# Performance work log

Hardware: AMD Instinct MI355X
Metric: run time of the kernel (lower is better)

## Reference

```python
import jax, jax.numpy as jnp
import numpy as np

B, D, A, H, NH = 32768, 768, 17, 128, 4
DH = H // NH


def _ln(x, g, b, eps=1e-5):
    mu = jnp.mean(x, axis=-1, keepdims=True)
    var = jnp.mean((x - mu) ** 2, axis=-1, keepdims=True)
    return (x - mu) / jnp.sqrt(var + eps) * g + b


def setup_inputs() -> dict:
    key = jax.random.key(0)
    ks = jax.random.split(key, 16)
    s = 0.02
    return {
        "visual_feat": jax.random.normal(ks[0], (B, D), jnp.float32),
        "au_feat": jax.random.uniform(ks[1], (B, A), jnp.float32),
        "w_tok": jax.random.normal(ks[2], (H, 1), jnp.float32) * s,
        "b_tok": jnp.zeros((H,), jnp.float32),
        "pos": jax.random.normal(ks[3], (1, A, H), jnp.float32) * s,
        "g_auln": jnp.ones((H,), jnp.float32),
        "b_auln": jnp.zeros((H,), jnp.float32),
        "w_q": jax.random.normal(ks[4], (H, D), jnp.float32) * s,
        "b_q": jnp.zeros((H,), jnp.float32),
        "w_in": jax.random.normal(ks[5], (3 * H, H), jnp.float32) * s,  # packed q,k,v in_proj
        "b_in": jnp.zeros((3 * H,), jnp.float32),
        "w_ao": jax.random.normal(ks[6], (H, H), jnp.float32) * s,  # MHA out_proj
        "b_ao": jnp.zeros((H,), jnp.float32),
        "g_aln": jnp.ones((H,), jnp.float32),
        "b_aln": jnp.zeros((H,), jnp.float32),
        "w_out": jax.random.normal(ks[7], (D, H), jnp.float32) * s,
        "b_out": jnp.zeros((D,), jnp.float32),
        "w_gate": jax.random.normal(ks[8], (D, 2 * D), jnp.float32) * s,
        "b_gate": jnp.zeros((D,), jnp.float32),
    }


def reference(visual_feat, au_feat, w_tok, b_tok, pos, g_auln, b_auln,
              w_q, b_q, w_in, b_in, w_ao, b_ao, g_aln, b_aln,
              w_out, b_out, w_gate, b_gate):
    # AU tokens: Linear(1 -> H) on intensities, + pos embed, LN. [B, A, H]
    au_tokens = au_feat[..., None] * w_tok[:, 0] + b_tok
    au_tokens = _ln(au_tokens + pos, g_auln, b_auln)
    # query: [B, H] (seq len 1)
    query = visual_feat @ w_q.T + b_q
    # MultiheadAttention (batch_first, packed in_proj)
    wq, wk, wv = w_in[:H], w_in[H:2 * H], w_in[2 * H:]
    bq, bk, bv = b_in[:H], b_in[H:2 * H], b_in[2 * H:]
    q = (query @ wq.T + bq).reshape(-1, NH, DH)          # [B, nh, dh]
    k = (au_tokens @ wk.T + bk).reshape(-1, A, NH, DH)   # [B, A, nh, dh]
    v = (au_tokens @ wv.T + bv).reshape(-1, A, NH, DH)
    scale = 1.0 / jnp.sqrt(jnp.asarray(DH, q.dtype))
    scores = jnp.einsum('bhd,bahd->bha', q * scale, k)   # [B, nh, A]
    attn = jax.nn.softmax(scores, axis=-1)
    ctx = jnp.einsum('bha,bahd->bhd', attn, v).reshape(-1, H)
    attn_out = ctx @ w_ao.T + b_ao
    attn_out = _ln(attn_out, g_aln, b_aln)
    attn_feat = attn_out @ w_out.T + b_out               # [B, D]
    gate_in = jnp.concatenate([visual_feat, attn_feat], axis=1)
    gate = jax.nn.sigmoid(gate_in @ w_gate.T + b_gate)
    return gate * attn_feat + (1.0 - gate) * visual_feat
```

## Files before the change

kernel.cpp:

```cpp
#include <hip/hip_runtime.h>
#include <hip/hip_bf16.h>

typedef __hip_bfloat16 bf16;
typedef __attribute__((ext_vector_type(8))) short short8;
typedef __attribute__((ext_vector_type(4))) float f32x4;
typedef __attribute__((ext_vector_type(8))) __bf16 bf16x8;

#define NB 32768
#define DD 768
#define AA 17
#define HH 128

__device__ __forceinline__ float bs2f(short s){
  unsigned int u = ((unsigned int)(unsigned short)s) << 16;
  return __builtin_bit_cast(float, u);
}
__device__ __forceinline__ short f2bs(float f){
  bf16 h = __float2bfloat16(f);
  return __builtin_bit_cast(short, h);
}
__device__ __forceinline__ f32x4 mfma16(short8 a, short8 b, f32x4 c){
  return __builtin_amdgcn_mfma_f32_16x16x32_bf16(
      __builtin_bit_cast(bf16x8, a), __builtin_bit_cast(bf16x8, b), c, 0, 0, 0);
}

template<int F32>
__device__ __forceinline__ short8 ldchunk(const void* base, long elem_off){
  if (F32){
    const float4* p = (const float4*)((const float*)base + elem_off);
    float4 x = p[0], y = p[1];
    short8 r;
    r[0]=f2bs(x.x); r[1]=f2bs(x.y); r[2]=f2bs(x.z); r[3]=f2bs(x.w);
    r[4]=f2bs(y.x); r[5]=f2bs(y.y); r[6]=f2bs(y.z); r[7]=f2bs(y.w);
    return r;
  } else {
    return *(const short8*)((const short*)base + elem_off);
  }
}


__device__ __forceinline__ float blk_mean128(float v, float* tmp){
  int t = threadIdx.x;
  #pragma unroll
  for (int m = 32; m; m >>= 1) v += __shfl_xor(v, m);
  if ((t & 63) == 0) tmp[t >> 6] = v;
  __syncthreads();
  float r = (tmp[0] + tmp[1]) * (1.0f / 128.0f);
  __syncthreads();
  return r;
}

__global__ void prep1(const float* __restrict__ w_tok, const float* __restrict__ b_tok,
                      const float* __restrict__ pos, const float* __restrict__ g_auln,
                      float* __restrict__ ug, float* __restrict__ rg, float* __restrict__ coef){
  __shared__ float tmp[2];
  int h = threadIdx.x;
  float w = w_tok[h];
  float wbar = blk_mean128(w, tmp);
  float u = w - wbar;
  float g = g_auln[h];
  ug[h] = u * g;
  float muu = blk_mean128(u * u, tmp);
  if (h == 0) coef[0] = muu;
  float bt = b_tok[h];
  for (int a = 0; a < AA; ++a){
    float c = bt + pos[a * HH + h];
    float cbar = blk_mean128(c, tmp);
    float r = c - cbar;
    rg[a * HH + h] = r * g;
    float mur = blk_mean128(u * r, tmp);
    float mrr = blk_mean128(r * r, tmp);
    if (h == 0){ coef[1 + a] = mur; coef[18 + a] = mrr; }
  }
}

__global__ void prep2(const float* __restrict__ w_in, const float* __restrict__ b_in,
                      const float* __restrict__ b_auln, const float* __restrict__ b_q,
                      const float* __restrict__ ug, const float* __restrict__ rg,
                      float* __restrict__ Uk, float* __restrict__ Ck,
                      float* __restrict__ Uv, float* __restrict__ Cv,
                      float* __restrict__ Rk, float* __restrict__ Rv,
                      float* __restrict__ bqf){
  int hp = threadIdx.x, bid = blockIdx.x;
  const float* wqrow = w_in + (long)hp * HH;
  const float* wkrow = w_in + (long)(HH + hp) * HH;
  const float* wvrow = w_in + (long)(2 * HH + hp) * HH;
  if (bid < AA){
    int a = bid;
    float sk = 0.f, sv = 0.f;
    for (int t = 0; t < HH; ++t){
      float r = rg[a * HH + t];
      sk += r * wkrow[t];
      sv += r * wvrow[t];
    }
    Rk[a * HH + hp] = sk; Rv[a * HH + hp] = sv;
  } else if (bid == AA){
    float uk = 0.f, uv = 0.f, ck = 0.f, cv = 0.f;
    for (int t = 0; t < HH; ++t){
      float u = ug[t], ba = b_auln[t];
      float wk = wkrow[t], wv = wvrow[t];
      uk += u * wk; uv += u * wv; ck += ba * wk; cv += ba * wv;
    }
    Uk[hp] = uk; Uv[hp] = uv;
    Ck[hp] = ck + b_in[HH + hp];
    Cv[hp] = cv + b_in[2 * HH + hp];
  } else {
    float s = 0.f;
    for (int t = 0; t < HH; ++t) s += b_q[t] * wqrow[t];
    bqf[hp] = s + b_in[hp];
  }
}

__global__ void prep_wqf(const float* __restrict__ w_in, const float* __restrict__ w_q,
                         bf16* __restrict__ Wqf){
  __shared__ float wq[HH];
  int h = blockIdx.x, t = threadIdx.x;
  if (t < HH) wq[t] = w_in[(long)h * HH + t];
  __syncthreads();
  for (int j = t; j < DD; j += 256){
    float acc = 0.f;
    for (int k = 0; k < HH; ++k) acc += wq[k] * w_q[(long)k * DD + j];
    Wqf[(long)h * DD + j] = __float2bfloat16(acc);
  }
}

__global__ void prep_gate(const float* __restrict__ w_gate, const float* __restrict__ b_gate,
                          const float* __restrict__ w_out, const float* __restrict__ b_out,
                          bf16* __restrict__ Wg1b, bf16* __restrict__ Wg2w,
                          bf16* __restrict__ Woutb, float* __restrict__ bgp){
  __shared__ float wg2[DD];
  __shared__ float red[2];
  int c = blockIdx.x, t = threadIdx.x;
  const float* wrow = w_gate + (long)c * (2 * DD);
  for (int j = t; j < DD; j += 128){
    Wg1b[(long)c * DD + j] = __float2bfloat16(wrow[j]);
    wg2[j] = wrow[DD + j];
  }
  __syncthreads();
  float acc = 0.f;
  for (int j = 0; j < DD; ++j) acc = fmaf(wg2[j], w_out[(long)j * HH + t], acc);
  Wg2w[(long)c * HH + t] = __float2bfloat16(acc);
  Woutb[(long)c * HH + t] = __float2bfloat16(w_out[(long)c * HH + t]);
  float pb = 0.f;
  for (int j = t; j < DD; j += 128) pb = fmaf(wg2[j], b_out[j], pb);
  #pragma unroll
  for (int m = 32; m; m >>= 1) pb += __shfl_xor(pb, m);
  if ((t & 63) == 0) red[t >> 6] = pb;
  __syncthreads();
  if (t == 0) bgp[c] = b_gate[c] + red[0] + red[1];
}

__global__ __launch_bounds__(128) void attn(
    const bf16* __restrict__ Q, const float* __restrict__ au, const float* __restrict__ coef,
    const float* __restrict__ Uk_, const float* __restrict__ Ck_,
    const float* __restrict__ Uv_, const float* __restrict__ Cv_,
    const float* __restrict__ Rk, const float* __restrict__ Rv,
    bf16* __restrict__ ctx){
  const int ROWS = 8;
  int h = threadIdx.x;
  long row0 = (long)blockIdx.x * ROWS;
  float Uk = Uk_[h], Ck = Ck_[h], Uv = Uv_[h], Cv = Cv_[h];
  float cA = coef[0];
  __shared__ float sa[ROWS * AA];
  for (int idx = h; idx < ROWS * AA; idx += 128)
    sa[idx] = au[row0 * AA + idx];
  __syncthreads();
  const float scale = 0.17677669529663689f;
  for (int r = 0; r < ROWS; ++r){
    long row = row0 + r;
    float q = __bfloat162float(Q[row * HH + h]);
    float sc[AA], vv[AA];
    #pragma unroll
    for (int a = 0; a < AA; ++a){
      float s = sa[r * AA + a];
      float var = fmaf(s * s, cA, fmaf(2.f * s, coef[1 + a], coef[18 + a]));
      float rinv = rsqrtf(fmaxf(var, 0.f) + 1e-5f);
      float kk = fmaf(s, Uk, Rk[a * HH + h]) * rinv + Ck;
      vv[a]    = fmaf(s, Uv, Rv[a * HH + h]) * rinv + Cv;
      float p = q * kk;
      p += __shfl_xor(p, 16); p += __shfl_xor(p, 8); p += __shfl_xor(p, 4);
      p += __shfl_xor(p, 2);  p += __shfl_xor(p, 1);
      sc[a] = p * scale;
    }
    float mx = sc[0];
    #pragma unroll
    for (int a = 1; a < AA; ++a) mx = fmaxf(mx, sc[a]);
    float den = 0.f, cval = 0.f;
    #pragma unroll
    for (int a = 0; a < AA; ++a){
      float e = __expf(sc[a] - mx);
      den += e; cval += e * vv[a];
    }
    ctx[row * HH + h] = __float2bfloat16(cval / den);
  }
}

template<int MODE, int AF, int BF, int SIDE>
__global__ __launch_bounds__(256) void gemm_bt(
    const void* __restrict__ A, long lda, int ks,
    const void* __restrict__ Bw, long ldb,
    const float* __restrict__ bias,
    const float* __restrict__ g_ln, const float* __restrict__ b_ln,
    short* __restrict__ sideA,
    bf16* __restrict__ C, long ldc)
{
  __shared__ __align__(16) short smem[128 * 136];
  short* As = smem;
  short* Bs = smem + 5120;
  const int tid = threadIdx.x;
  const int w = tid >> 6, l = tid & 63;
  const long rowBase = (long)blockIdx.y * 128;
  const int colBase = blockIdx.x * 128;
  const int fr = l & 15;
  const int kq = l >> 4;
  const int sr0 = tid >> 2,         sp0 = (tid & 3) * 8;
  const int sr1 = (tid + 256) >> 2;

  f32x4 acc[2][8];
  f32x4 zero = {0.f, 0.f, 0.f, 0.f};
  #pragma unroll
  for (int i = 0; i < 2; ++i)
    #pragma unroll
    for (int j = 0; j < 8; ++j) acc[i][j] = zero;

  for (int kt = 0; kt < ks; ++kt){
    const long kA = (long)kt * 32;
    short8 av0 = ldchunk<AF>(A, (rowBase + sr0) * lda + kA + sp0);
    short8 av1 = ldchunk<AF>(A, (rowBase + sr1) * lda + kA + sp0);
    short8 bv0 = ldchunk<BF>(Bw, (long)(colBase + sr0) * ldb + kA + sp0);
    short8 bv1 = ldchunk<BF>(Bw, (long)(colBase + sr1) * ldb + kA + sp0);
    if (SIDE){
      *(short8*)(sideA + (rowBase + sr0) * lda + kA + sp0) = av0;
      *(short8*)(sideA + (rowBase + sr1) * lda + kA + sp0) = av1;
    }
    __syncthreads();
    *(short8*)(As + sr0 * 40 + sp0) = av0;
    *(short8*)(As + sr1 * 40 + sp0) = av1;
    *(short8*)(Bs + sr0 * 40 + sp0) = bv0;
    *(short8*)(Bs + sr1 * 40 + sp0) = bv1;
    __syncthreads();
    const int ra0 = w * 32 + fr;
    short8 a0 = *(const short8*)(As + ra0 * 40 + kq * 8);
    short8 a1 = *(const short8*)(As + (ra0 + 16) * 40 + kq * 8);
    #pragma unroll
    for (int nt = 0; nt < 8; ++nt){
      short8 b = *(const short8*)(Bs + (nt * 16 + fr) * 40 + kq * 8);
      acc[0][nt] = mfma16(a0, b, acc[0][nt]);
      acc[1][nt] = mfma16(a1, b, acc[1][nt]);
    }
  }
  __syncthreads();

  short* ep = smem;
  if (MODE == 1){
    #pragma unroll
    for (int mt = 0; mt < 2; ++mt){
      #pragma unroll
      for (int r = 0; r < 4; ++r){
        float x[8]; float sm = 0.f, sq = 0.f;
        #pragma unroll
        for (int nt = 0; nt < 8; ++nt){
          const int col = colBase + nt * 16 + fr;
          x[nt] = acc[mt][nt][r] + bias[col];
          sm += x[nt]; sq += x[nt] * x[nt];
        }
        sm += __shfl_xor(sm, 1); sq += __shfl_xor(sq, 1);
        sm += __shfl_xor(sm, 2); sq += __shfl_xor(sq, 2);
        sm += __shfl_xor(sm, 4); sq += __shfl_xor(sq, 4);
        sm += __shfl_xor(sm, 8); sq += __shfl_xor(sq, 8);
        const float mu = sm * (1.f / 128.f);
        const float var = sq * (1.f / 128.f) - mu * mu;
        const float rinv = rsqrtf(fmaxf(var, 0.f) + 1e-5f);
        const int lrow = w * 32 + mt * 16 + kq * 4 + r;
        #pragma unroll
        for (int nt = 0; nt < 8; ++nt){
          const int col = colBase + nt * 16 + fr;
          float y = (x[nt] - mu) * rinv * g_ln[col] + b_ln[col];
          ep[lrow * 136 + nt * 16 + fr] = f2bs(y);
        }
      }
    }
  } else {
    #pragma unroll
    for (int nt = 0; nt < 8; ++nt){
      const int col = colBase + nt * 16 + fr;
      const float bv = bias[col];
      #pragma unroll
      for (int mt = 0; mt < 2; ++mt){
        const int lrow0 = w * 32 + mt * 16 + kq * 4;
        #pragma unroll
        for (int r = 0; r < 4; ++r)
          ep[(lrow0 + r) * 136 + nt * 16 + fr] = f2bs(acc[mt][nt][r] + bv);
      }
    }
  }
  __syncthreads();

  #pragma unroll
  for (int it = 0; it < 8; ++it){
    const int cid = tid + it * 256;
    const int rw = cid >> 4;
    const int cc = (cid & 15) * 8;
    const long gr = rowBase + rw;
    short8 vls = *(const short8*)(ep + rw * 136 + cc);
    short* cp = (short*)C + gr * ldc + colBase + cc;
    *(short8*)cp = vls;
  }
}

template<int A1F>
__global__ __launch_bounds__(256) void gemm_final(
    const void* __restrict__ A1,
    const bf16* __restrict__ aon,
    const bf16* __restrict__ Wg1b,
    const bf16* __restrict__ Wg2w,
    const bf16* __restrict__ Woutb,
    const float* __restrict__ bgp,
    const float* __restrict__ b_out,
    const float* __restrict__ vf,
    float* __restrict__ C)
{
  __shared__ __align__(16) short As[128 * 40];
  __shared__ __align__(16) short Bs[128 * 40];
  __shared__ __align__(16) short Bs2[128 * 40];
  const int tid = threadIdx.x;
  const int w = tid >> 6, l = tid & 63;
  const long rowBase = (long)blockIdx.y * 128;
  const int colBase = blockIdx.x * 128;
  const int fr = l & 15;
  const int kq = l >> 4;
  const int sr0 = tid >> 2,         sp0 = (tid & 3) * 8;
  const int sr1 = (tid + 256) >> 2;

  f32x4 accG[2][8], accF[2][8];
  f32x4 zero = {0.f, 0.f, 0.f, 0.f};
  #pragma unroll
  for (int i = 0; i < 2; ++i)
    #pragma unroll
    for (int j = 0; j < 8; ++j){ accG[i][j] = zero; accF[i][j] = zero; }

  for (int kt = 0; kt < DD / 32; ++kt){
    const long kA = (long)kt * 32;
    short8 av0 = ldchunk<A1F>(A1, (rowBase + sr0) * DD + kA + sp0);
    short8 av1 = ldchunk<A1F>(A1, (rowBase + sr1) * DD + kA + sp0);
    short8 bv0 = *(const short8*)((const short*)Wg1b + (long)(colBase + sr0) * DD + kA + sp0);
    short8 bv1 = *(const short8*)((const short*)Wg1b + (long)(colBase + sr1) * DD + kA + sp0);
    __syncthreads();
    *(short8*)(As + sr0 * 40 + sp0) = av0;
    *(short8*)(As + sr1 * 40 + sp0) = av1;
    *(short8*)(Bs + sr0 * 40 + sp0) = bv0;
    *(short8*)(Bs + sr1 * 40 + sp0) = bv1;
    __syncthreads();
    const int ra0 = w * 32 + fr;
    short8 a0 = *(const short8*)(As + ra0 * 40 + kq * 8);
    short8 a1 = *(const short8*)(As + (ra0 + 16) * 40 + kq * 8);
    #pragma unroll
    for (int nt = 0; nt < 8; ++nt){
      short8 b = *(const short8*)(Bs + (nt * 16 + fr) * 40 + kq * 8);
      accG[0][nt] = mfma16(a0, b, accG[0][nt]);
      accG[1][nt] = mfma16(a1, b, accG[1][nt]);
    }
  }

  for (int kt = 0; kt < HH / 32; ++kt){
    const long kA = (long)kt * 32;
    short8 av0 = *(const short8*)((const short*)aon + (rowBase + sr0) * HH + kA + sp0);
    short8 av1 = *(const short8*)((const short*)aon + (rowBase + sr1) * HH + kA + sp0);
    short8 bv0 = *(const short8*)((const short*)Wg2w + (long)(colBase + sr0) * HH + kA + sp0);
    short8 bv1 = *(const short8*)((const short*)Wg2w + (long)(colBase + sr1) * HH + kA + sp0);
    short8 cv0 = *(const short8*)((const short*)Woutb + (long)(colBase + sr0) * HH + kA + sp0);
    short8 cv1 = *(const short8*)((const short*)Woutb + (long)(colBase + sr1) * HH + kA + sp0);
    __syncthreads();
    *(short8*)(As + sr0 * 40 + sp0) = av0;
    *(short8*)(As + sr1 * 40 + sp0) = av1;
    *(short8*)(Bs + sr0 * 40 + sp0) = bv0;
    *(short8*)(Bs + sr1 * 40 + sp0) = bv1;
    *(short8*)(Bs2 + sr0 * 40 + sp0) = cv0;
    *(short8*)(Bs2 + sr1 * 40 + sp0) = cv1;
    __syncthreads();
    const int ra0 = w * 32 + fr;
    short8 a0 = *(const short8*)(As + ra0 * 40 + kq * 8);
    short8 a1 = *(const short8*)(As + (ra0 + 16) * 40 + kq * 8);
    #pragma unroll
    for (int nt = 0; nt < 8; ++nt){
      short8 b  = *(const short8*)(Bs  + (nt * 16 + fr) * 40 + kq * 8);
      short8 b2 = *(const short8*)(Bs2 + (nt * 16 + fr) * 40 + kq * 8);
      accG[0][nt] = mfma16(a0, b,  accG[0][nt]);
      accG[1][nt] = mfma16(a1, b,  accG[1][nt]);
      accF[0][nt] = mfma16(a0, b2, accF[0][nt]);
      accF[1][nt] = mfma16(a1, b2, accF[1][nt]);
    }
  }

  float bg[8], bo[8];
  #pragma unroll
  for (int nt = 0; nt < 8; ++nt){
    const int col = colBase + nt * 16 + fr;
    bg[nt] = bgp[col];
    bo[nt] = b_out[col];
  }
  #pragma unroll
  for (int mt = 0; mt < 2; ++mt){
    const long r0 = rowBase + w * 32 + mt * 16 + kq * 4;
    #pragma unroll
    for (int r = 0; r < 4; ++r){
      const long row = r0 + r;
      const float* vrow = vf + row * DD;
      float* crow = C + row * DD;
      #pragma unroll
      for (int nt = 0; nt < 8; ++nt){
        const int col = colBase + nt * 16 + fr;
        const float lin = accG[mt][nt][r] + bg[nt];
        const float afv = accF[mt][nt][r] + bo[nt];
        const float gate = 1.f / (1.f + __expf(-lin));
        crow[col] = gate * afv + (1.f - gate) * vrow[col];
      }
    }
  }
}

extern "C" void kernel_launch(void* const* d_in, const int* in_sizes, int n_in,
                              void* d_out, int out_size, void* d_ws, size_t ws_size,
                              hipStream_t stream){
  const float* visual = (const float*)d_in[0];
  const float* au     = (const float*)d_in[1];
  const float* w_tok  = (const float*)d_in[2];
  const float* b_tok  = (const float*)d_in[3];
  const float* pos    = (const float*)d_in[4];
  const float* g_auln = (const float*)d_in[5];
  const float* b_auln = (const float*)d_in[6];
  const float* w_q    = (const float*)d_in[7];
  const float* b_q    = (const float*)d_in[8];
  const float* w_in   = (const float*)d_in[9];
  const float* b_in   = (const float*)d_in[10];
  const float* w_ao   = (const float*)d_in[11];
  const float* b_ao   = (const float*)d_in[12];
  const float* g_aln  = (const float*)d_in[13];
  const float* b_aln  = (const float*)d_in[14];
  const float* w_out  = (const float*)d_in[15];
  const float* b_out  = (const float*)d_in[16];
  const float* w_gate = (const float*)d_in[17];
  const float* b_gate = (const float*)d_in[18];

  char* ob = (char*)d_out;
  bf16* Q   = (bf16*)(ob);
  bf16* ctx = (bf16*)(ob + ((size_t)8 << 20));
  char* p = ob + ((size_t)16 << 20);
  auto alloc = [&](size_t bytes){ char* r = p; p += (bytes + 255) & ~(size_t)255; return r; };
  bf16*  Wqf  = (bf16*) alloc((size_t)HH * DD * 2);
  float* bqf  = (float*)alloc(HH * 4);
  float* ug   = (float*)alloc(HH * 4);
  float* rg   = (float*)alloc(AA * HH * 4);
  float* coef = (float*)alloc(64 * 4);
  float* Uk   = (float*)alloc(HH * 4);
  float* Ck   = (float*)alloc(HH * 4);
  float* Uv   = (float*)alloc(HH * 4);
  float* Cv   = (float*)alloc(HH * 4);
  float* Rk   = (float*)alloc(AA * HH * 4);
  float* Rv   = (float*)alloc(AA * HH * 4);

  char* q = (char*)d_ws;
  auto walloc = [&](size_t bytes){ char* r = q; q += (bytes + 255) & ~(size_t)255; return r; };
  bf16*  aon   = (bf16*) walloc((size_t)NB * HH * 2);
  bf16*  Wg1b  = (bf16*) walloc((size_t)DD * DD * 2);
  bf16*  Wg2w  = (bf16*) walloc((size_t)DD * HH * 2);
  bf16*  Woutb = (bf16*) walloc((size_t)DD * HH * 2);
  float* bgp   = (float*)walloc(DD * 4);
  bf16*  vbf   = (bf16*) walloc((size_t)NB * DD * 2);
  const bool use_vbf = (size_t)(q - (char*)d_ws) <= ws_size;

  prep1<<<dim3(1), dim3(128), 0, stream>>>(w_tok, b_tok, pos, g_auln, ug, rg, coef);
  prep2<<<dim3(19), dim3(128), 0, stream>>>(w_in, b_in, b_auln, b_q, ug, rg, Uk, Ck, Uv, Cv, Rk, Rv, bqf);
  prep_wqf<<<dim3(128), dim3(256), 0, stream>>>(w_in, w_q, Wqf);
  prep_gate<<<dim3(DD), dim3(128), 0, stream>>>(w_gate, b_gate, w_out, b_out, Wg1b, Wg2w, Woutb, bgp);

  if (use_vbf)
    gemm_bt<0, 1, 0, 1><<<dim3(1, NB / 128), dim3(256), 0, stream>>>(
        visual, (long)DD, DD / 32, Wqf, (long)DD,
        bqf, nullptr, nullptr, (short*)vbf, Q, (long)HH);
  else
    gemm_bt<0, 1, 0, 0><<<dim3(1, NB / 128), dim3(256), 0, stream>>>(
        visual, (long)DD, DD / 32, Wqf, (long)DD,
        bqf, nullptr, nullptr, nullptr, Q, (long)HH);

  attn<<<dim3(NB / 8), dim3(128), 0, stream>>>(Q, au, coef, Uk, Ck, Uv, Cv, Rk, Rv, ctx);

  gemm_bt<1, 0, 1, 0><<<dim3(1, NB / 128), dim3(256), 0, stream>>>(
      ctx, (long)HH, HH / 32, w_ao, (long)HH,
      b_ao, g_aln, b_aln, nullptr, aon, (long)HH);

  if (use_vbf)
    gemm_final<0><<<dim3(DD / 128, NB / 128), dim3(256), 0, stream>>>(
        vbf, aon, Wg1b, Wg2w, Woutb, bgp, b_out, visual, (float*)d_out);
  else
    gemm_final<1><<<dim3(DD / 128, NB / 128), dim3(256), 0, stream>>>(
        visual, aon, Wg1b, Wg2w, Woutb, bgp, b_out, visual, (float*)d_out);
}
```

Baseline: 532.7 us.

## Double-buffer LDS tiles in GEMM kernels and add XCD-aware block swizzle

Both GEMM kernels now use two LDS tile buffers. Each iteration prefetches the next K-slice from global memory into registers while MFMAs run on the current buffer, then writes the prefetched data into the other buffer, so only one barrier is needed per iteration instead of two. This is meant to hide global-load latency behind compute. gemm_final also remaps block IDs so that blocks dispatched round-robin to the same XCD cover contiguous rows, which should improve L2 reuse of A rows. In exchange it uses more LDS and registers, which may lower occupancy.

```diff
diff --git a/kernel.cpp b/kernel.cpp
--- a/kernel.cpp
+++ b/kernel.cpp
@@ -204,9 +204,7 @@
     short* __restrict__ sideA,
     bf16* __restrict__ C, long ldc)
 {
-  __shared__ __align__(16) short smem[128 * 136];
-  short* As = smem;
-  short* Bs = smem + 5120;
+  __shared__ __align__(16) short smem[20480];
   const int tid = threadIdx.x;
   const int w = tid >> 6, l = tid & 63;
   const long rowBase = (long)blockIdx.y * 128;
@@ -223,30 +221,52 @@
     #pragma unroll
     for (int j = 0; j < 8; ++j) acc[i][j] = zero;
 
+  {
+    short8 av0 = ldchunk<AF>(A, (rowBase + sr0) * lda + sp0);
+    short8 av1 = ldchunk<AF>(A, (rowBase + sr1) * lda + sp0);
+    short8 bv0 = ldchunk<BF>(Bw, (long)(colBase + sr0) * ldb + sp0);
+    short8 bv1 = ldchunk<BF>(Bw, (long)(colBase + sr1) * ldb + sp0);
+    if (SIDE){
+      *(short8*)(sideA + (rowBase + sr0) * lda + sp0) = av0;
+      *(short8*)(sideA + (rowBase + sr1) * lda + sp0) = av1;
+    }
+    *(short8*)(smem + sr0 * 40 + sp0) = av0;
+    *(short8*)(smem + sr1 * 40 + sp0) = av1;
+    *(short8*)(smem + 5120 + sr0 * 40 + sp0) = bv0;
+    *(short8*)(smem + 5120 + sr1 * 40 + sp0) = bv1;
+  }
+
   for (int kt = 0; kt < ks; ++kt){
-    const long kA = (long)kt * 32;
-    short8 av0 = ldchunk<AF>(A, (rowBase + sr0) * lda + kA + sp0);
-    short8 av1 = ldchunk<AF>(A, (rowBase + sr1) * lda + kA + sp0);
-    short8 bv0 = ldchunk<BF>(Bw, (long)(colBase + sr0) * ldb + kA + sp0);
-    short8 bv1 = ldchunk<BF>(Bw, (long)(colBase + sr1) * ldb + kA + sp0);
-    if (SIDE){
-      *(short8*)(sideA + (rowBase + sr0) * lda + kA + sp0) = av0;
-      *(short8*)(sideA + (rowBase + sr1) * lda + kA + sp0) = av1;
-    }
     __syncthreads();
-    *(short8*)(As + sr0 * 40 + sp0) = av0;
-    *(short8*)(As + sr1 * 40 + sp0) = av1;
-    *(short8*)(Bs + sr0 * 40 + sp0) = bv0;
-    *(short8*)(Bs + sr1 * 40 + sp0) = bv1;
-    __syncthreads();
+    short* cb = smem + (kt & 1) * 10240;
+    short* nb = smem + ((kt + 1) & 1) * 10240;
+    const bool pf = (kt + 1 < ks);
+    short8 av0, av1, bv0, bv1;
+    if (pf){
+      const long kA = (long)(kt + 1) * 32;
+      av0 = ldchunk<AF>(A, (rowBase + sr0) * lda + kA + sp0);
+      av1 = ldchunk<AF>(A, (rowBase + sr1) * lda + kA + sp0);
+      bv0 = ldchunk<BF>(Bw, (long)(colBase + sr0) * ldb + kA + sp0);
+      bv1 = ldchunk<BF>(Bw, (long)(colBase + sr1) * ldb + kA + sp0);
+      if (SIDE){
+        *(short8*)(sideA + (rowBase + sr0) * lda + kA + sp0) = av0;
+        *(short8*)(sideA + (rowBase + sr1) * lda + kA + sp0) = av1;
+      }
+    }
     const int ra0 = w * 32 + fr;
-    short8 a0 = *(const short8*)(As + ra0 * 40 + kq * 8);
-    short8 a1 = *(const short8*)(As + (ra0 + 16) * 40 + kq * 8);
+    short8 a0 = *(const short8*)(cb + ra0 * 40 + kq * 8);
+    short8 a1 = *(const short8*)(cb + (ra0 + 16) * 40 + kq * 8);
     #pragma unroll
     for (int nt = 0; nt < 8; ++nt){
-      short8 b = *(const short8*)(Bs + (nt * 16 + fr) * 40 + kq * 8);
+      short8 b = *(const short8*)(cb + 5120 + (nt * 16 + fr) * 40 + kq * 8);
       acc[0][nt] = mfma16(a0, b, acc[0][nt]);
       acc[1][nt] = mfma16(a1, b, acc[1][nt]);
+    }
+    if (pf){
+      *(short8*)(nb + sr0 * 40 + sp0) = av0;
+      *(short8*)(nb + sr1 * 40 + sp0) = av1;
+      *(short8*)(nb + 5120 + sr0 * 40 + sp0) = bv0;
+      *(short8*)(nb + 5120 + sr1 * 40 + sp0) = bv1;
     }
   }
   __syncthreads();
@@ -320,13 +340,17 @@
     const float* __restrict__ vf,
     float* __restrict__ C)
 {
-  __shared__ __align__(16) short As[128 * 40];
-  __shared__ __align__(16) short Bs[128 * 40];
-  __shared__ __align__(16) short Bs2[128 * 40];
+  __shared__ __align__(16) short smem[20480];
   const int tid = threadIdx.x;
   const int w = tid >> 6, l = tid & 63;
-  const long rowBase = (long)blockIdx.y * 128;
-  const int colBase = blockIdx.x * 128;
+
+  const int nx = 6;
+  const int bid = blockIdx.y * nx + blockIdx.x;
+  const int cpx = (NB / 128) * nx / 8;
+  const int swz = (bid & 7) * cpx + (bid >> 3);
+  const long rowBase = (long)(swz / nx) * 128;
+  const int colBase = (swz % nx) * 128;
+
   const int fr = l & 15;
   const int kq = l >> 4;
   const int sr0 = tid >> 2,         sp0 = (tid & 3) * 8;
@@ -339,29 +363,49 @@
     #pragma unroll
     for (int j = 0; j < 8; ++j){ accG[i][j] = zero; accF[i][j] = zero; }
 
+  {
+    short8 av0 = ldchunk<A1F>(A1, (rowBase + sr0) * DD + sp0);
+    short8 av1 = ldchunk<A1F>(A1, (rowBase + sr1) * DD + sp0);
+    short8 bv0 = *(const short8*)((const short*)Wg1b + (long)(colBase + sr0) * DD + sp0);
+    short8 bv1 = *(const short8*)((const short*)Wg1b + (long)(colBase + sr1) * DD + sp0);
+    *(short8*)(smem + sr0 * 40 + sp0) = av0;
+    *(short8*)(smem + sr1 * 40 + sp0) = av1;
+    *(short8*)(smem + 5120 + sr0 * 40 + sp0) = bv0;
+    *(short8*)(smem + 5120 + sr1 * 40 + sp0) = bv1;
+  }
   for (int kt = 0; kt < DD / 32; ++kt){
-    const long kA = (long)kt * 32;
-    short8 av0 = ldchunk<A1F>(A1, (rowBase + sr0) * DD + kA + sp0);
-    short8 av1 = ldchunk<A1F>(A1, (rowBase + sr1) * DD + kA + sp0);
-    short8 bv0 = *(const short8*)((const short*)Wg1b + (long)(colBase + sr0) * DD + kA + sp0);
-    short8 bv1 = *(const short8*)((const short*)Wg1b + (long)(colBase + sr1) * DD + kA + sp0);
     __syncthreads();
-    *(short8*)(As + sr0 * 40 + sp0) = av0;
-    *(short8*)(As + sr1 * 40 + sp0) = av1;
-    *(short8*)(Bs + sr0 * 40 + sp0) = bv0;
-    *(short8*)(Bs + sr1 * 40 + sp0) = bv1;
-    __syncthreads();
+    short* cb = smem + (kt & 1) * 10240;
+    short* nb = smem + ((kt + 1) & 1) * 10240;
+    const bool pf = (kt + 1 < DD / 32);
+    short8 av0, av1, bv0, bv1;
+    if (pf){
+      const long kA = (long)(kt + 1) * 32;
+      av0 = ldchunk<A1F>(A1, (rowBase + sr0) * DD + kA + sp0);
+      av1 = ldchunk<A1F>(A1, (rowBase + sr1) * DD + kA + sp0);
+      bv0 = *(const short8*)((const short*)Wg1b + (long)(colBase + sr0) * DD + kA + sp0);
+      bv1 = *(const short8*)((const short*)Wg1b + (long)(colBase + sr1) * DD + kA + sp0);
+    }
     const int ra0 = w * 32 + fr;
-    short8 a0 = *(const short8*)(As + ra0 * 40 + kq * 8);
-    short8 a1 = *(const short8*)(As + (ra0 + 16) * 40 + kq * 8);
+    short8 a0 = *(const short8*)(cb + ra0 * 40 + kq * 8);
+    short8 a1 = *(const short8*)(cb + (ra0 + 16) * 40 + kq * 8);
     #pragma unroll
     for (int nt = 0; nt < 8; ++nt){
-      short8 b = *(const short8*)(Bs + (nt * 16 + fr) * 40 + kq * 8);
+      short8 b = *(const short8*)(cb + 5120 + (nt * 16 + fr) * 40 + kq * 8);
       accG[0][nt] = mfma16(a0, b, accG[0][nt]);
       accG[1][nt] = mfma16(a1, b, accG[1][nt]);
     }
-  }
-
+    if (pf){
+      *(short8*)(nb + sr0 * 40 + sp0) = av0;
+      *(short8*)(nb + sr1 * 40 + sp0) = av1;
+      *(short8*)(nb + 5120 + sr0 * 40 + sp0) = bv0;
+      *(short8*)(nb + 5120 + sr1 * 40 + sp0) = bv1;
+    }
+  }
+
+  short* As = smem;
+  short* Bs = smem + 5120;
+  short* Bs2 = smem + 10240;
   for (int kt = 0; kt < HH / 32; ++kt){
     const long kA = (long)kt * 32;
     short8 av0 = *(const short8*)((const short*)aon + (rowBase + sr0) * HH + kA + sp0);
```

After: 578.0 us. +8.5%, slower.
